# Performance work log

Hardware: AMD Instinct MI355X
Metric: run time of the kernel (lower is better)

Reference implementation:

```python
import jax, jax.numpy as jnp
import numpy as np

B, S, D, H = 2, 2048, 2048, 16
HD = D // H  # 128


def _rope_tables(seq_len, dim, base=10000.0):
    inv_freq = 1.0 / (base ** (jnp.arange(0, dim, 2, dtype=jnp.float32) / dim))
    t = jnp.arange(seq_len, dtype=jnp.float32)
    freqs = jnp.outer(t, inv_freq)  # [S, dim/2]
    return jnp.cos(freqs), jnp.sin(freqs)


def _apply_rotary(x, cos, sin):
    # x: [B, S, H, HD]; cos/sin: [S, HD/2] -> broadcast [1, S, 1, HD/2]
    half = x.shape[-1] // 2
    x1, x2 = x[..., :half], x[..., half:]
    c = cos[None, :, None, :]
    s = sin[None, :, None, :]
    return jnp.concatenate([x1 * c - x2 * s, x1 * s + x2 * c], axis=-1)


def setup_inputs() -> dict:
    key = jax.random.key(0)
    ks = jax.random.split(key, 5)
    x = jax.random.normal(ks[0], (B, S, D), dtype=jnp.float32)
    Wq = jax.random.normal(ks[1], (D, D), dtype=jnp.float32) * 0.02
    Wk = jax.random.normal(ks[2], (D, D), dtype=jnp.float32) * 0.02
    Wv = jax.random.normal(ks[3], (D, D), dtype=jnp.float32) * 0.02
    Wo = jax.random.normal(ks[4], (D, D), dtype=jnp.float32) * 0.02
    mask = jnp.tril(jnp.ones((S, S), dtype=jnp.int32))[None, None]  # [1,1,S,S] causal
    return {"x": x, "mask": mask, "Wq": Wq, "Wk": Wk, "Wv": Wv, "Wo": Wo}


def reference(x, mask, Wq, Wk, Wv, Wo):
    b, s, d = x.shape
    # nn.Linear(bias=False): y = x @ W.T
    q = (x @ Wq.T).reshape(b, s, H, HD)
    k = (x @ Wk.T).reshape(b, s, H, HD)
    v = (x @ Wv.T).reshape(b, s, H, HD)
    cos, sin = _rope_tables(s, HD)
    q = _apply_rotary(q, cos, sin)
    k = _apply_rotary(k, cos, sin)
    # -> [B, H, S, HD]
    q = q.transpose(0, 2, 1, 3)
    k = k.transpose(0, 2, 1, 3)
    v = v.transpose(0, 2, 1, 3)
    scores = jnp.einsum('bhqd,bhkd->bhqk', q, k) / jnp.sqrt(jnp.float32(HD))
    scores = jnp.where(mask == 0, -jnp.inf, scores)
    attn = jax.nn.softmax(scores, axis=-1)
    out = jnp.einsum('bhqk,bhkd->bhqd', attn, v)
    out = out.transpose(0, 2, 1, 3).reshape(b, s, d)
    return out @ Wo.T
```

## Files before the change

kernel.cpp:

```cpp
#include <hip/hip_runtime.h>
#include <hip/hip_bf16.h>

typedef __attribute__((ext_vector_type(8))) short short8;
typedef __attribute__((ext_vector_type(4))) short s4;
typedef __attribute__((ext_vector_type(4))) float f32x4;

#define S_TOK 2048

__device__ __forceinline__ float b2f(ushort u) {
  union { unsigned i; float f; } v; v.i = ((unsigned)u) << 16; return v.f;
}
__device__ __forceinline__ ushort f2b(float f) {
  __hip_bfloat16 h = __float2bfloat16(f);
  union { __hip_bfloat16 h; ushort u; } v; v.h = h; return v.u;
}

__device__ __forceinline__ void async_load16(const void* g, void* l) {
  __builtin_amdgcn_global_load_lds(
      (const __attribute__((address_space(1))) unsigned int*)g,
      (__attribute__((address_space(3))) unsigned int*)l, 16, 0, 0);
}

__device__ const int QT_OF[40] = {0,1,2,3, 4,4,5,5,6,6,7,7, 8,8,8,9,9,9,10,10,10,11,11,11,
                                  12,12,12,12,13,13,13,13,14,14,14,14,15,15,15,15};
__device__ const int C_OF[40]  = {0,0,0,0, 0,1,0,1,0,1,0,1, 0,1,2,0,1,2,0,1,2,0,1,2,
                                  0,1,2,3,0,1,2,3,0,1,2,3,0,1,2,3};
__device__ const int S0_OF[16] = {0,1,2,3,4,6,8,10,12,15,18,21,24,28,32,36};
__device__ const int NC_OF[16] = {1,1,1,1,2,2,2,2,3,3,3,3,4,4,4,4};

__global__ __launch_bounds__(256) void cvt_f32_bf16(const float* __restrict__ in,
                                                    ushort* __restrict__ out, int n) {
  int i = (blockIdx.x * 256 + threadIdx.x) * 4;
  if (i < n) {
    float4 v = *(const float4*)(in + i);
    ushort4 o;
    o.x = f2b(v.x); o.y = f2b(v.y); o.z = f2b(v.z); o.w = f2b(v.w);
    *(ushort4*)(out + i) = o;
  }
}

__global__ __launch_bounds__(256) void cvt_w4(const float* __restrict__ w0,
                                              const float* __restrict__ w1,
                                              const float* __restrict__ w2,
                                              const float* __restrict__ w3,
                                              ushort* __restrict__ out, int n) {
  const float* src = blockIdx.y == 0 ? w0 : blockIdx.y == 1 ? w1 : blockIdx.y == 2 ? w2 : w3;
  int i = (blockIdx.x * 256 + threadIdx.x) * 4;
  if (i < n) {
    float4 v = *(const float4*)(src + i);
    ushort4 o;
    o.x = f2b(v.x); o.y = f2b(v.y); o.z = f2b(v.z); o.w = f2b(v.w);
    *(ushort4*)(out + (size_t)blockIdx.y * n + i) = o;
  }
}

template <bool OUTF32>
__global__ __launch_bounds__(256) void gemm_bt(const ushort* __restrict__ A,
                                               const ushort* __restrict__ Bw,
                                               void* __restrict__ Cv,
                                               int lda, int ldb, int ldc) {
  __shared__ __align__(16) ushort As[128 * 32];
  __shared__ __align__(16) ushort Bs[128 * 32];
  const int tid  = threadIdx.x;
  const int lane = tid & 63;
  const int w    = tid >> 6;
  const int quad = lane >> 4;
  const int l15  = lane & 15;
  const int m0 = blockIdx.x * 128;
  const int n0 = blockIdx.y * 128;
  const int wm = (w & 1) * 64;
  const int wn = (w >> 1) * 64;

  f32x4 acc[4][4];
  #pragma unroll
  for (int i = 0; i < 4; ++i)
    #pragma unroll
    for (int j = 0; j < 4; ++j) acc[i][j] = (f32x4){0.f, 0.f, 0.f, 0.f};

  for (int k0 = 0; k0 < 2048; k0 += 32) {
    #pragma unroll
    for (int j = 0; j < 2; ++j) {
      int s = tid + j * 256;
      int row = s >> 2, qp = s & 3;
      int kof = (qp ^ ((row >> 1) & 3)) * 8;
      async_load16(A  + (size_t)(m0 + row) * lda + k0 + kof, &As[s * 8]);
      async_load16(Bw + (size_t)(n0 + row) * ldb + k0 + kof, &Bs[s * 8]);
    }
    __syncthreads();
    short8 af[4], bf[4];
    #pragma unroll
    for (int mi = 0; mi < 4; ++mi) {
      int row = wm + mi * 16 + l15;
      af[mi] = *(const short8*)&As[(row * 4 + (quad ^ ((row >> 1) & 3))) * 8];
    }
    #pragma unroll
    for (int ni = 0; ni < 4; ++ni) {
      int row = wn + ni * 16 + l15;
      bf[ni] = *(const short8*)&Bs[(row * 4 + (quad ^ ((row >> 1) & 3))) * 8];
    }
    #pragma unroll
    for (int mi = 0; mi < 4; ++mi)
      #pragma unroll
      for (int ni = 0; ni < 4; ++ni)
        acc[mi][ni] = __builtin_amdgcn_mfma_f32_16x16x32_bf16(af[mi], bf[ni], acc[mi][ni], 0, 0, 0);
    __syncthreads();
  }

  #pragma unroll
  for (int mi = 0; mi < 4; ++mi)
    #pragma unroll
    for (int ni = 0; ni < 4; ++ni)
      #pragma unroll
      for (int r = 0; r < 4; ++r) {
        int rr = m0 + wm + mi * 16 + quad * 4 + r;
        int cc = n0 + wn + ni * 16 + l15;
        if constexpr (OUTF32)
          ((float*)Cv)[(size_t)rr * ldc + cc] = acc[mi][ni][r];
        else
          ((ushort*)Cv)[(size_t)rr * ldc + cc] = f2b(acc[mi][ni][r]);
      }
}

__global__ __launch_bounds__(256) void gemm_qk(const ushort* __restrict__ A,
                                               const ushort* __restrict__ W0,
                                               const ushort* __restrict__ W1,
                                               ushort* __restrict__ C) {
  __shared__ __align__(16) ushort As[128 * 32];
  __shared__ __align__(16) ushort Bs[128 * 32];
  const int wsel = blockIdx.y >> 4;
  const ushort* Bw = wsel == 0 ? W0 : W1;
  const int tid  = threadIdx.x;
  const int lane = tid & 63;
  const int w    = tid >> 6;
  const int quad = lane >> 4;
  const int l15  = lane & 15;
  const int m0 = blockIdx.x * 128;
  const int n0 = (blockIdx.y & 15) * 128;
  const int wm = (w & 1) * 64;
  const int wn = (w >> 1) * 64;

  f32x4 acc[4][4];
  #pragma unroll
  for (int i = 0; i < 4; ++i)
    #pragma unroll
    for (int j = 0; j < 4; ++j) acc[i][j] = (f32x4){0.f, 0.f, 0.f, 0.f};

  for (int k0 = 0; k0 < 2048; k0 += 32) {
    #pragma unroll
    for (int j = 0; j < 2; ++j) {
      int s = tid + j * 256;
      int row = s >> 2, qp = s & 3;
      int kof = (qp ^ ((row >> 1) & 3)) * 8;
      async_load16(A  + (size_t)(m0 + row) * 2048 + k0 + kof, &As[s * 8]);
      async_load16(Bw + (size_t)(n0 + row) * 2048 + k0 + kof, &Bs[s * 8]);
    }
    __syncthreads();
    short8 af[4], bf[4];
    #pragma unroll
    for (int mi = 0; mi < 4; ++mi) {
      int row = wm + mi * 16 + l15;
      af[mi] = *(const short8*)&As[(row * 4 + (quad ^ ((row >> 1) & 3))) * 8];
    }
    #pragma unroll
    for (int ni = 0; ni < 4; ++ni) {
      int row = wn + ni * 16 + l15;
      bf[ni] = *(const short8*)&Bs[(row * 4 + (quad ^ ((row >> 1) & 3))) * 8];
    }
    #pragma unroll
    for (int mi = 0; mi < 4; ++mi)
      #pragma unroll
      for (int ni = 0; ni < 4; ++ni)
        acc[mi][ni] = __builtin_amdgcn_mfma_f32_16x16x32_bf16(af[mi], bf[ni], acc[mi][ni], 0, 0, 0);
    __syncthreads();
  }

  ushort* Cb = C + wsel * 2048;
  #pragma unroll
  for (int mi = 0; mi < 4; ++mi)
    #pragma unroll
    for (int ni = 0; ni < 4; ++ni)
      #pragma unroll
      for (int r = 0; r < 4; ++r) {
        int rr = m0 + wm + mi * 16 + quad * 4 + r;
        int cc = n0 + wn + ni * 16 + l15;
        Cb[(size_t)rr * 4096 + cc] = f2b(acc[mi][ni][r]);
      }
}

__global__ __launch_bounds__(256) void rope_k(ushort* __restrict__ QK) {
  const int t = blockIdx.x * 256 + threadIdx.x;
  const int j = t & 63;
  const int h = (t >> 6) & 15;
  const int row = t >> 10;
  const int pos = row & (S_TOK - 1);
  const float invf = __expf(-0.14391156831212787f * (float)j);
  const float ph = (float)pos * invf;
  float sn, cs;
  __sincosf(ph, &sn, &cs);
  size_t base = (size_t)row * 4096 + h * 128 + j;
  float x1 = b2f(QK[base]);
  float x2 = b2f(QK[base + 64]);
  QK[base]      = f2b(x1 * cs - x2 * sn);
  QK[base + 64] = f2b(x1 * sn + x2 * cs);
  float y1 = b2f(QK[base + 2048]);
  float y2 = b2f(QK[base + 2048 + 64]);
  QK[base + 2048]      = f2b(y1 * cs - y2 * sn);
  QK[base + 2048 + 64] = f2b(y1 * sn + y2 * cs);
}

__global__ __launch_bounds__(256, 2) void attn_chunk(const ushort* __restrict__ QK,
                                                     const ushort* __restrict__ Vt,
                                                     ushort* __restrict__ Opart,
                                                     float* __restrict__ Ml) {
  __shared__ __align__(16) ushort Ks[2][8192];
  __shared__ __align__(16) ushort Vs[2][8192];
  const int s = blockIdx.x, h = blockIdx.y, b = blockIdx.z;
  const int qt = QT_OF[s], c = C_OF[s];
  const int q0 = qt * 128;
  const int t0 = c * 8, tend = min(t0 + 8, 2 * qt + 2);
  const int slot = (b * 16 + h) * 40 + s;
  const int tid = threadIdx.x, lane = tid & 63, w = tid >> 6;
  const int quad = lane >> 4, l15 = lane & 15;
  const size_t rowbase = (size_t)b * S_TOK;
  const float scale = 0.08838834764831845f;

  short8 qf[2][4];
  #pragma unroll
  for (int m = 0; m < 2; ++m)
    #pragma unroll
    for (int ks = 0; ks < 4; ++ks)
      qf[m][ks] = *(const short8*)(QK + (rowbase + q0 + w * 32 + m * 16 + l15) * 4096
                                   + h * 128 + ks * 32 + quad * 8);

  f32x4 o[2][8];
  #pragma unroll
  for (int m = 0; m < 2; ++m)
    #pragma unroll
    for (int no = 0; no < 8; ++no) o[m][no] = (f32x4){0.f, 0.f, 0.f, 0.f};
  float lsum[2] = {0.f, 0.f};

  auto issue_k = [&](int t, int buf) {
    const ushort* kb = QK + (rowbase + (size_t)t * 64) * 4096 + 2048 + h * 128;
    #pragma unroll
    for (int i = 0; i < 4; ++i) {
      int sl = tid + i * 256;
      int row = sl >> 4, cs = sl & 15;
      async_load16(kb + (size_t)row * 4096 + (cs ^ (row & 15)) * 8, &Ks[buf][sl * 8]);
    }
  };
  auto issue_v = [&](int t, int buf) {
    const ushort* vb = Vt + (size_t)(h * 128) * 4096 + b * S_TOK + (size_t)t * 64;
    #pragma unroll
    for (int i = 0; i < 4; ++i) {
      int sl = tid + i * 256;
      int hd = sl >> 3, cc = (sl & 7) ^ (hd & 7);
      async_load16(vb + (size_t)hd * 4096 + cc * 8, &Vs[buf][sl * 8]);
    }
  };

  issue_k(t0, 0);
  issue_v(t0, 0);

  for (int t = t0; t < tend; ++t) {
    const int buf = (t - t0) & 1;
    __syncthreads();
    if (t + 1 < tend) { issue_k(t + 1, buf ^ 1); issue_v(t + 1, buf ^ 1); }

    const ushort* KsT = Ks[buf];
    const ushort* VsT = Vs[buf];
    const bool domask = (t * 64 + 64 > q0);

    #pragma unroll
    for (int n = 0; n < 4; ++n) {
      short8 kf[4];
      #pragma unroll
      for (int ks = 0; ks < 4; ++ks) {
        int row = n * 16 + l15;
        kf[ks] = *(const short8*)&KsT[(row * 16 + ((ks * 4 + quad) ^ (row & 15))) * 8];
      }
      s4 pfm[2];
      #pragma unroll
      for (int m = 0; m < 2; ++m) {
        f32x4 z = (f32x4){0.f, 0.f, 0.f, 0.f};
        #pragma unroll
        for (int ks = 0; ks < 4; ++ks)
          z = __builtin_amdgcn_mfma_f32_16x16x32_bf16(kf[ks], qf[m][ks], z, 0, 0, 0);
        const int qg = q0 + w * 32 + m * 16 + l15;
        float p[4];
        #pragma unroll
        for (int r = 0; r < 4; ++r) {
          int kvg = t * 64 + n * 16 + quad * 4 + r;
          float pv = __expf(z[r] * scale);
          if (domask && kvg > qg) pv = 0.f;
          p[r] = pv;
          lsum[m] += pv;
        }
        s4 pk;
        pk[0] = (short)f2b(p[0]); pk[1] = (short)f2b(p[1]);
        pk[2] = (short)f2b(p[2]); pk[3] = (short)f2b(p[3]);
        pfm[m] = pk;
      }
      #pragma unroll
      for (int no = 0; no < 8; ++no) {
        int hd = no * 16 + l15;
        int cc = 2 * n + (quad >> 1);
        s4 vf = *(const s4*)&VsT[(hd * 8 + (cc ^ (hd & 7))) * 8 + (quad & 1) * 4];
        #pragma unroll
        for (int m = 0; m < 2; ++m)
          o[m][no] = __builtin_amdgcn_mfma_f32_16x16x16bf16_1k(pfm[m], vf, o[m][no], 0, 0, 0);
      }
    }
  }

  #pragma unroll
  for (int m = 0; m < 2; ++m) {
    lsum[m] += __shfl_xor(lsum[m], 16);
    lsum[m] += __shfl_xor(lsum[m], 32);
  }
  if (quad == 0) {
    #pragma unroll
    for (int m = 0; m < 2; ++m)
      Ml[(size_t)slot * 128 + w * 32 + m * 16 + l15] = lsum[m];
  }

  __syncthreads();
  ushort* Es = &Ks[0][w * 2048];
  ushort* Op = Opart + (size_t)slot * 16384;
  #pragma unroll
  for (int m = 0; m < 2; ++m) {
    #pragma unroll
    for (int no = 0; no < 8; ++no)
      #pragma unroll
      for (int r = 0; r < 4; ++r)
        Es[(quad * 4 + r) * 128 + no * 16 + l15] = f2b(o[m][no][r]);
    __asm__ volatile("s_waitcnt lgkmcnt(0)" ::: "memory");
    #pragma unroll
    for (int j = 0; j < 4; ++j) {
      int cchunk = lane * 4 + j;
      int row_l = cchunk >> 4, colc = cchunk & 15;
      short8 vv = *(const short8*)&Es[row_l * 128 + colc * 8];
      *(short8*)(Op + (size_t)(w * 32 + m * 16 + row_l) * 128 + colc * 8) = vv;
    }
    __asm__ volatile("s_waitcnt lgkmcnt(0)" ::: "memory");
  }
}

__global__ __launch_bounds__(256) void attn_combine(const ushort* __restrict__ Opart,
                                                    const float* __restrict__ Ml,
                                                    ushort* __restrict__ Ob) {
  const int qt = blockIdx.x, h = blockIdx.y, b = blockIdx.z;
  const int nc = NC_OF[qt];
  const int base = (b * 16 + h) * 40 + S0_OF[qt];
  const int tid = threadIdx.x;
  const int row = tid >> 1, half = tid & 1;

  float l = 0.f;
  for (int c = 0; c < nc; ++c) l += Ml[(size_t)(base + c) * 128 + row];
  const float inv_l = 1.f / l;

  float acc[64];
  #pragma unroll
  for (int i = 0; i < 64; ++i) acc[i] = 0.f;
  for (int c = 0; c < nc; ++c) {
    const ushort* Op = Opart + (size_t)(base + c) * 16384 + row * 128 + half * 64;
    #pragma unroll
    for (int k = 0; k < 8; ++k) {
      short8 v = *(const short8*)(Op + k * 8);
      #pragma unroll
      for (int u = 0; u < 8; ++u) acc[k * 8 + u] += b2f((ushort)v[u]);
    }
  }

  ushort* dst = Ob + ((size_t)(b * S_TOK + qt * 128 + row)) * 2048 + h * 128 + half * 64;
  #pragma unroll
  for (int k = 0; k < 8; ++k) {
    short8 ov;
    #pragma unroll
    for (int u = 0; u < 8; ++u) ov[u] = (short)f2b(acc[k * 8 + u] * inv_l);
    *(short8*)(dst + k * 8) = ov;
  }
}

extern "C" void kernel_launch(void* const* d_in, const int* in_sizes, int n_in,
                              void* d_out, int out_size, void* d_ws, size_t ws_size,
                              hipStream_t stream) {
  const float* x  = (const float*)d_in[0];
  const float* Wq = (const float*)d_in[2];
  const float* Wk = (const float*)d_in[3];
  const float* Wv = (const float*)d_in[4];
  const float* Wo = (const float*)d_in[5];
  float* out = (float*)d_out;

  ushort* xb    = (ushort*)d_ws;
  ushort* Wb    = xb + (size_t)4096 * 2048;
  ushort* QK    = Wb + (size_t)4 * 2048 * 2048;
  ushort* Vt    = QK + (size_t)4096 * 4096;
  ushort* Opart = Vt + (size_t)2048 * 4096;
  float*  Ml    = (float*)(Opart + (size_t)1280 * 16384);
  ushort* Ob    = xb;

  const int NX = 4096 * 2048;
  const int NW = 2048 * 2048;
  dim3 blk(256);

  cvt_f32_bf16<<<dim3(NX / 1024), blk, 0, stream>>>(x, xb, NX);
  cvt_w4<<<dim3(NW / 1024, 4), blk, 0, stream>>>(Wq, Wk, Wv, Wo, Wb, NW);

  gemm_qk<<<dim3(32, 32), blk, 0, stream>>>(xb, Wb, Wb + (size_t)NW, QK);
  gemm_bt<false><<<dim3(16, 32), blk, 0, stream>>>(Wb + (size_t)2 * NW, xb, Vt, 2048, 2048, 4096);
  rope_k<<<dim3(16384), blk, 0, stream>>>(QK);
  attn_chunk<<<dim3(40, 16, 2), blk, 0, stream>>>(QK, Vt, Opart, Ml);
  attn_combine<<<dim3(16, 16, 2), blk, 0, stream>>>(Opart, Ml, Ob);
  gemm_bt<true><<<dim3(32, 16), blk, 0, stream>>>(Ob, Wb + (size_t)3 * NW, out, 2048, 2048, 2048);
}
```

Measured before the change: 437.2 us.

## Replace projection GEMMs with 256x256-tile, 4-stage pipelined 512-thread kernel

Replaces the 128x128 double-sync GEMM kernels with a single 256x256-tile kernel using 8 waves. It keeps a 4-deep LDS ring of async global-to-LDS loads, issuing each stage three iterations ahead with explicit vmcnt waits. It splits each k-step into two MFMA halves, with barriers and s_setprio around the math. The Q/K projection is merged into one launch by treating Wq and Wk as one 4096-row weight. The aim is to hide global load latency and halve operand refetch per output, at the cost of 128KB of LDS, one block per CU, and only 128 blocks for the V and output GEMMs on a 256-CU part.

```diff
diff --git a/kernel.cpp b/kernel.cpp
--- a/kernel.cpp
+++ b/kernel.cpp
@@ -19,6 +19,12 @@
   __builtin_amdgcn_global_load_lds(
       (const __attribute__((address_space(1))) unsigned int*)g,
       (__attribute__((address_space(3))) unsigned int*)l, 16, 0, 0);
+}
+
+__device__ __forceinline__ void wg_barrier() {
+  __asm__ volatile("" ::: "memory");
+  __builtin_amdgcn_s_barrier();
+  __asm__ volatile("" ::: "memory");
 }
 
 __device__ const int QT_OF[40] = {0,1,2,3, 4,4,5,5,6,6,7,7, 8,8,8,9,9,9,10,10,10,11,11,11,
@@ -55,59 +61,96 @@
 }
 
 template <bool OUTF32>
-__global__ __launch_bounds__(256) void gemm_bt(const ushort* __restrict__ A,
-                                               const ushort* __restrict__ Bw,
-                                               void* __restrict__ Cv,
-                                               int lda, int ldb, int ldc) {
-  __shared__ __align__(16) ushort As[128 * 32];
-  __shared__ __align__(16) ushort Bs[128 * 32];
+__global__ __launch_bounds__(512, 2) void gemm256(const ushort* __restrict__ A,
+                                                  const ushort* __restrict__ Bw,
+                                                  void* __restrict__ Cv,
+                                                  int lda, int ldb, int ldc) {
+  __shared__ __align__(16) ushort As[4][256 * 32];
+  __shared__ __align__(16) ushort Bs[4][256 * 32];
   const int tid  = threadIdx.x;
   const int lane = tid & 63;
   const int w    = tid >> 6;
   const int quad = lane >> 4;
   const int l15  = lane & 15;
-  const int m0 = blockIdx.x * 128;
-  const int n0 = blockIdx.y * 128;
-  const int wm = (w & 1) * 64;
+  const int m0 = blockIdx.x * 256;
+  const int n0 = blockIdx.y * 256;
+  const int wm = (w & 1) * 128;
   const int wn = (w >> 1) * 64;
 
-  f32x4 acc[4][4];
-  #pragma unroll
-  for (int i = 0; i < 4; ++i)
+  f32x4 acc[8][4];
+  #pragma unroll
+  for (int i = 0; i < 8; ++i)
     #pragma unroll
     for (int j = 0; j < 4; ++j) acc[i][j] = (f32x4){0.f, 0.f, 0.f, 0.f};
 
-  for (int k0 = 0; k0 < 2048; k0 += 32) {
-    #pragma unroll
-    for (int j = 0; j < 2; ++j) {
-      int s = tid + j * 256;
-      int row = s >> 2, qp = s & 3;
-      int kof = (qp ^ ((row >> 1) & 3)) * 8;
-      async_load16(A  + (size_t)(m0 + row) * lda + k0 + kof, &As[s * 8]);
-      async_load16(Bw + (size_t)(n0 + row) * ldb + k0 + kof, &Bs[s * 8]);
-    }
-    __syncthreads();
-    short8 af[4], bf[4];
+  auto stage = [&](int t, int j) {
+    const int r = t & 3;
+    const int s = tid + j * 512;
+    const int row = s >> 2, qp = s & 3;
+    const int kof = (qp ^ ((row >> 1) & 3)) * 8;
+    const int k0 = t * 32;
+    async_load16(A  + (size_t)(m0 + row) * lda + k0 + kof, &As[r][s * 8]);
+    async_load16(Bw + (size_t)(n0 + row) * ldb + k0 + kof, &Bs[r][s * 8]);
+  };
+
+  stage(0, 0); stage(0, 1);
+  stage(1, 0); stage(1, 1);
+  stage(2, 0); stage(2, 1);
+  __asm__ volatile("s_waitcnt vmcnt(8)" ::: "memory");
+  wg_barrier();
+
+  constexpr int nT = 64;
+  #pragma unroll 1
+  for (int u = 0; u < nT; ++u) {
+    const ushort* At = As[u & 3];
+    const ushort* Bt = Bs[u & 3];
+    short8 afr[4], bfr[4];
+
+    #pragma unroll
+    for (int ni = 0; ni < 4; ++ni) {
+      int row = wn + ni * 16 + l15;
+      bfr[ni] = *(const short8*)&Bt[(row * 4 + (quad ^ ((row >> 1) & 3))) * 8];
+    }
     #pragma unroll
     for (int mi = 0; mi < 4; ++mi) {
       int row = wm + mi * 16 + l15;
-      af[mi] = *(const short8*)&As[(row * 4 + (quad ^ ((row >> 1) & 3))) * 8];
-    }
-    #pragma unroll
-    for (int ni = 0; ni < 4; ++ni) {
-      int row = wn + ni * 16 + l15;
-      bf[ni] = *(const short8*)&Bs[(row * 4 + (quad ^ ((row >> 1) & 3))) * 8];
-    }
+      afr[mi] = *(const short8*)&At[(row * 4 + (quad ^ ((row >> 1) & 3))) * 8];
+    }
+    if (u + 3 < nT) stage(u + 3, 0);
+    wg_barrier();
+    __asm__ volatile("s_waitcnt lgkmcnt(0)" ::: "memory");
+    __builtin_amdgcn_s_setprio(1);
     #pragma unroll
     for (int mi = 0; mi < 4; ++mi)
       #pragma unroll
       for (int ni = 0; ni < 4; ++ni)
-        acc[mi][ni] = __builtin_amdgcn_mfma_f32_16x16x32_bf16(af[mi], bf[ni], acc[mi][ni], 0, 0, 0);
-    __syncthreads();
-  }
-
-  #pragma unroll
-  for (int mi = 0; mi < 4; ++mi)
+        acc[mi][ni] = __builtin_amdgcn_mfma_f32_16x16x32_bf16(afr[mi], bfr[ni], acc[mi][ni], 0, 0, 0);
+    __builtin_amdgcn_s_setprio(0);
+    wg_barrier();
+
+    #pragma unroll
+    for (int mi = 0; mi < 4; ++mi) {
+      int row = wm + 64 + mi * 16 + l15;
+      afr[mi] = *(const short8*)&At[(row * 4 + (quad ^ ((row >> 1) & 3))) * 8];
+    }
+    if (u + 3 < nT) stage(u + 3, 1);
+    wg_barrier();
+    __asm__ volatile("s_waitcnt lgkmcnt(0)" ::: "memory");
+    __builtin_amdgcn_s_setprio(1);
+    #pragma unroll
+    for (int mi = 0; mi < 4; ++mi)
+      #pragma unroll
+      for (int ni = 0; ni < 4; ++ni)
+        acc[4 + mi][ni] = __builtin_amdgcn_mfma_f32_16x16x32_bf16(afr[mi], bfr[ni], acc[4 + mi][ni], 0, 0, 0);
+    __builtin_amdgcn_s_setprio(0);
+    if (u + 3 < nT)      { __asm__ volatile("s_waitcnt vmcnt(8)" ::: "memory"); }
+    else if (u + 2 < nT) { __asm__ volatile("s_waitcnt vmcnt(4)" ::: "memory"); }
+    else if (u + 1 < nT) { __asm__ volatile("s_waitcnt vmcnt(0)" ::: "memory"); }
+    wg_barrier();
+  }
+
+  #pragma unroll
+  for (int mi = 0; mi < 8; ++mi)
     #pragma unroll
     for (int ni = 0; ni < 4; ++ni)
       #pragma unroll
@@ -118,72 +161,6 @@
           ((float*)Cv)[(size_t)rr * ldc + cc] = acc[mi][ni][r];
         else
           ((ushort*)Cv)[(size_t)rr * ldc + cc] = f2b(acc[mi][ni][r]);
-      }
-}
-
-__global__ __launch_bounds__(256) void gemm_qk(const ushort* __restrict__ A,
-                                               const ushort* __restrict__ W0,
-                                               const ushort* __restrict__ W1,
-                                               ushort* __restrict__ C) {
-  __shared__ __align__(16) ushort As[128 * 32];
-  __shared__ __align__(16) ushort Bs[128 * 32];
-  const int wsel = blockIdx.y >> 4;
-  const ushort* Bw = wsel == 0 ? W0 : W1;
-  const int tid  = threadIdx.x;
-  const int lane = tid & 63;
-  const int w    = tid >> 6;
-  const int quad = lane >> 4;
-  const int l15  = lane & 15;
-  const int m0 = blockIdx.x * 128;
-  const int n0 = (blockIdx.y & 15) * 128;
-  const int wm = (w & 1) * 64;
-  const int wn = (w >> 1) * 64;
-
-  f32x4 acc[4][4];
-  #pragma unroll
-  for (int i = 0; i < 4; ++i)
-    #pragma unroll
-    for (int j = 0; j < 4; ++j) acc[i][j] = (f32x4){0.f, 0.f, 0.f, 0.f};
-
-  for (int k0 = 0; k0 < 2048; k0 += 32) {
-    #pragma unroll
-    for (int j = 0; j < 2; ++j) {
-      int s = tid + j * 256;
-      int row = s >> 2, qp = s & 3;
-      int kof = (qp ^ ((row >> 1) & 3)) * 8;
-      async_load16(A  + (size_t)(m0 + row) * 2048 + k0 + kof, &As[s * 8]);
-      async_load16(Bw + (size_t)(n0 + row) * 2048 + k0 + kof, &Bs[s * 8]);
-    }
-    __syncthreads();
-    short8 af[4], bf[4];
-    #pragma unroll
-    for (int mi = 0; mi < 4; ++mi) {
-      int row = wm + mi * 16 + l15;
-      af[mi] = *(const short8*)&As[(row * 4 + (quad ^ ((row >> 1) & 3))) * 8];
-    }
-    #pragma unroll
-    for (int ni = 0; ni < 4; ++ni) {
-      int row = wn + ni * 16 + l15;
-      bf[ni] = *(const short8*)&Bs[(row * 4 + (quad ^ ((row >> 1) & 3))) * 8];
-    }
-    #pragma unroll
-    for (int mi = 0; mi < 4; ++mi)
-      #pragma unroll
-      for (int ni = 0; ni < 4; ++ni)
-        acc[mi][ni] = __builtin_amdgcn_mfma_f32_16x16x32_bf16(af[mi], bf[ni], acc[mi][ni], 0, 0, 0);
-    __syncthreads();
-  }
-
-  ushort* Cb = C + wsel * 2048;
-  #pragma unroll
-  for (int mi = 0; mi < 4; ++mi)
-    #pragma unroll
-    for (int ni = 0; ni < 4; ++ni)
-      #pragma unroll
-      for (int r = 0; r < 4; ++r) {
-        int rr = m0 + wm + mi * 16 + quad * 4 + r;
-        int cc = n0 + wn + ni * 16 + l15;
-        Cb[(size_t)rr * 4096 + cc] = f2b(acc[mi][ni][r]);
       }
 }
 
@@ -402,14 +379,15 @@
   const int NX = 4096 * 2048;
   const int NW = 2048 * 2048;
   dim3 blk(256);
+  dim3 blk512(512);
 
   cvt_f32_bf16<<<dim3(NX / 1024), blk, 0, stream>>>(x, xb, NX);
   cvt_w4<<<dim3(NW / 1024, 4), blk, 0, stream>>>(Wq, Wk, Wv, Wo, Wb, NW);
 
-  gemm_qk<<<dim3(32, 32), blk, 0, stream>>>(xb, Wb, Wb + (size_t)NW, QK);
-  gemm_bt<false><<<dim3(16, 32), blk, 0, stream>>>(Wb + (size_t)2 * NW, xb, Vt, 2048, 2048, 4096);
+  gemm256<false><<<dim3(16, 16), blk512, 0, stream>>>(xb, Wb, QK, 2048, 2048, 4096);
+  gemm256<false><<<dim3(8, 16), blk512, 0, stream>>>(Wb + (size_t)2 * NW, xb, Vt, 2048, 2048, 4096);
   rope_k<<<dim3(16384), blk, 0, stream>>>(QK);
   attn_chunk<<<dim3(40, 16, 2), blk, 0, stream>>>(QK, Vt, Opart, Ml);
   attn_combine<<<dim3(16, 16, 2), blk, 0, stream>>>(Opart, Ml, Ob);
-  gemm_bt<true><<<dim3(32, 16), blk, 0, stream>>>(Ob, Wb + (size_t)3 * NW, out, 2048, 2048, 2048);
-}
+  gemm256<true><<<dim3(16, 8), blk512, 0, stream>>>(Ob, Wb + (size_t)3 * NW, out, 2048, 2048, 2048);
+}
```

New measurement: 446.8 us. 1.02x slower.
